# Performance work log

Measured on AMD Instinct MI355X. Metric: run time of the kernel, lower is better.

## Reference

```python
import jax, jax.numpy as jnp
import numpy as np
import math

# BilateralDenoiser(influence=1.0): sigma = max(1.0*2, 1e-4) = 2.0
SIGMA = 2.0
RAD = math.ceil(SIGMA * 2.5)   # 5 -> 11x11 window (N = 2*RAD+1)
EPS = 1e-4
B, H, W = 1, 1080, 1920


def setup_inputs() -> dict:
    key = jax.random.key(0)
    # [B,H,W,8] = color(3) | normal(3) | z(1) | dz(1); rand keeps z,dz positive
    x = jax.random.uniform(key, (B, H, W, 8), dtype=jnp.float32)
    return {"input": x}


def _denoise(inp):
    col = inp[..., 0:3]
    n = inp[..., 3:6]
    # util.safe_normalize: x / sqrt(clamp(dot(x,x), min=1e-20))
    nrm = n * jax.lax.rsqrt(jnp.clip(jnp.sum(n * n, -1, keepdims=True), 1e-20, None))
    z = inp[..., 6:7]
    dz = inp[..., 7:8]

    pad = ((0, 0), (RAD, RAD), (RAD, RAD), (0, 0))
    col_p = jnp.pad(col, pad)
    nrm_p = jnp.pad(nrm, pad)
    z_p = jnp.pad(z, pad)
    m_p = jnp.pad(jnp.ones_like(z), pad)  # validity mask: out-of-image taps get w=0
    var = jnp.float32(SIGMA * SIGMA)

    def row(carry, dy):
        acc_c, acc_w = carry
        for dx in range(-RAD, RAD + 1):  # fixed 11-wide unroll, vectorized over B,H,W
            start = (0, dy + RAD, dx + RAD, 0)
            t_c = jax.lax.dynamic_slice(col_p, start, (B, H, W, 3))
            t_n = jax.lax.dynamic_slice(nrm_p, start, (B, H, W, 3))
            t_z = jax.lax.dynamic_slice(z_p, start, (B, H, W, 1))
            t_m = jax.lax.dynamic_slice(m_p, start, (B, H, W, 1))
            d2 = (dy * dy + dx * dx).astype(jnp.float32)
            w_xy = jnp.exp(-d2 / (2.0 * var))                      # spatial gaussian
            w_n = jnp.clip(jnp.sum(t_n * nrm, -1, keepdims=True), 0.0, 1.0) ** 128  # normal similarity
            w_d = jnp.exp(-jnp.abs(t_z - z) / jnp.maximum(dz * jnp.sqrt(d2), EPS))  # depth similarity
            wgt = w_xy * w_n * w_d * t_m
            acc_c = acc_c + t_c * wgt
            acc_w = acc_w + wgt
        return (acc_c, acc_w), None

    dys = jnp.arange(-RAD, RAD + 1, dtype=jnp.int32)
    init = (jnp.zeros_like(col), jnp.zeros_like(z))
    (s_c, s_w), _ = jax.lax.scan(row, init, dys)
    # center tap always has weight 1 -> s_w >= 1, safe division
    return s_c / s_w


def reference(input):
    return _denoise(input)
```

## Files before the change

kernel.cpp:

```cpp
#include <hip/hip_runtime.h>
#include <math.h>

#define HH 1080
#define WW 1920
#define RAD 5
#define TX 32
#define TY 16
#define RPT 2
#define BDY 8
#define LR (TY + 2*RAD)
#define LC (TX + 2*RAD)

__device__ __forceinline__ float fast_rcp(float x) {
#if __has_builtin(__builtin_amdgcn_rcpf)
    return __builtin_amdgcn_rcpf(x);
#else
    return 1.0f / x;
#endif
}
__device__ __forceinline__ float fast_rsq(float x) {
#if __has_builtin(__builtin_amdgcn_rsqf)
    return __builtin_amdgcn_rsqf(x);
#else
    return rsqrtf(x);
#endif
}
__device__ __forceinline__ float fast_exp2(float x) {
#if __has_builtin(__builtin_amdgcn_exp2f)
    return __builtin_amdgcn_exp2f(x);
#else
    return exp2f(x);
#endif
}


__global__ __launch_bounds__(TX*BDY, 4)
void denoise_kernel(const float* __restrict__ in, float* __restrict__ out) {
    __shared__ float4 sA[LR][LC];
    __shared__ float2 sN[LR][LC];
    __shared__ float  sZ[LR][LC];

    const int tx = threadIdx.x;
    const int ty = threadIdx.y;
    const int tid = ty * TX + tx;
    const int x0 = blockIdx.x * TX;
    const int y0 = blockIdx.y * TY;

    #pragma unroll
    for (int i = 0; i < (LR * LC + TX * BDY - 1) / (TX * BDY); ++i) {
        int idx = tid + i * (TX * BDY);
        if (idx < LR * LC) {
            int r = idx / LC, c = idx % LC;
            int gx = x0 + c - RAD;
            int gy = y0 + r - RAD;
            float4 a = make_float4(0.f, 0.f, 0.f, 0.f);
            float4 b = make_float4(0.f, 0.f, 0.f, 0.f);
            if ((unsigned)gx < (unsigned)WW && (unsigned)gy < (unsigned)HH) {
                const float4* p = reinterpret_cast<const float4*>(in + ((size_t)gy * WW + gx) * 8);
                a = p[0];
                b = p[1];
            }
            float nn = a.w * a.w + b.x * b.x + b.y * b.y;
            float s = fast_rsq(fmaxf(nn, 1e-20f));
            sA[r][c] = make_float4(a.x, a.y, a.z, a.w * s);
            sN[r][c] = make_float2(b.x * s, b.y * s);
            sZ[r][c] = b.z;
        }
    }
    __syncthreads();

    float cn0[RPT], cn1[RPT], cn2[RPT], cz[RPT], rdz[RPT];
    #pragma unroll
    for (int o = 0; o < RPT; ++o) {
        int rr = ty * RPT + RAD + o, cc = tx + RAD;
        float4 A = sA[rr][cc];
        float2 N = sN[rr][cc];
        cn0[o] = A.w; cn1[o] = N.x; cn2[o] = N.y; cz[o] = sZ[rr][cc];
        int gy = y0 + ty * RPT + o;
        float dzv = 1.0f;
        if (gy < HH) dzv = in[(((size_t)gy * WW) + (x0 + tx)) * 8 + 7];
        rdz[o] = fminf(1.4426950408889634f * fast_rcp(dzv), 1e10f);
    }
    const float rr1 = rdz[1] * fast_rcp(rdz[0]);

    float accx[RPT] = {0.f, 0.f};
    float accy[RPT] = {0.f, 0.f};
    float accz[RPT] = {0.f, 0.f};
    float accw[RPT] = {0.f, 0.f};

    float tmu0[RAD + 1] = {}, tmu1[RAD + 1] = {};

    #define ROW_BODY(CHECK)                                                          \
    {                                                                                \
        _Pragma("unroll")                                                            \
        for (int k = 0; k <= RAD; ++k) tmu1[k] = tmu0[k] * rr1;                      \
        if (!CHECK || r <= 2 * RAD) {   \
            int dy0 = r - RAD;                                                      \
            float dy0sq = (float)(dy0 * dy0);                                       \
            _Pragma("unroll")                                                       \
            for (int k = 0; k <= RAD; ++k)                                          \
                tmu0[k] = rdz[0] * fast_rsq(dy0sq + (float)(k * k));                \
        }                                                                            \
        float tmv[RPT][RAD + 1], cxv[RPT][RAD + 1];                                  \
        bool  val[RPT];                                                              \
        _Pragma("unroll")                                                            \
        for (int o = 0; o < RPT; ++o) {                                              \
            int dy = r - RAD - o;                                                    \
            val[o] = (dy >= -RAD) && (dy <= RAD);                                    \
            if (!CHECK || val[o]) {                                                  \
                float dy2f = (float)(dy * dy);                                       \
                float bneg = fmaf(dy2f, -0.18033688011112042f, -276.997447850681f);  \
                _Pragma("unroll")                                                    \
                for (int k = 0; k <= RAD; ++k) {                                     \
                    float tmuk = (o == 0) ? tmu0[k] : tmu1[k];                       \
                    cxv[o][k] = bneg + (float)(k * k) * -0.18033688011112042f;       \
                    tmv[o][k] = fminf(tmuk, 14426.950408889634f);                    \
                }                                                                    \
            }                                                                        \
        }                                                                            \
        _Pragma("unroll")                                                            \
        for (int dx = 0; dx < 2 * RAD + 1; ++dx) {                                   \
            float4 A  = sA[ty * RPT + r][tx + dx];                                   \
            float2 N  = sN[ty * RPT + r][tx + dx];                                   \
            float  tz = sZ[ty * RPT + r][tx + dx];                                   \
            const int k = (dx < RAD) ? (RAD - dx) : (dx - RAD);                      \
            _Pragma("unroll")                                                        \
            for (int o = 0; o < RPT; ++o) {                                          \
                if (!CHECK || val[o]) {                                              \
                    float dot = fmaf(A.w, cn0[o], fmaf(N.x, cn1[o], N.y * cn2[o]));  \
                    float vv  = fmaf(dot, -92.332482616893665f, 369.32993046757466f); \
                    float zd  = tz - cz[o];                                          \
                    float e2a = fmaf(-fabsf(zd), tmv[o][k], cxv[o][k]);              \
                    float e2  = fmaf(dot, vv, e2a);                                  \
                    float w   = fast_exp2(e2);                                       \
                    accx[o] = fmaf(A.x, w, accx[o]);                                 \
                    accy[o] = fmaf(A.y, w, accy[o]);                                 \
                    accz[o] = fmaf(A.z, w, accz[o]);                                 \
                    accw[o] += w;                                                    \
                }                                                                    \
            }                                                                        \
        }                                                                            \
    }

    #pragma unroll 1
    for (int r = 0; r < RPT - 1; ++r) ROW_BODY(true)
    #pragma unroll 1
    for (int r = RPT - 1; r <= 2 * RAD; ++r) ROW_BODY(false)
    #pragma unroll 1
    for (int r = 2 * RAD + 1; r < 2 * RAD + RPT; ++r) ROW_BODY(true)

    #undef ROW_BODY

    const int xo = x0 + tx;
    #pragma unroll
    for (int o = 0; o < RPT; ++o) {
        int y = y0 + ty * RPT + o;
        if (y < HH) {
            float inv = fast_rcp(accw[o]);
            size_t base = ((size_t)y * WW + xo) * 3;
            out[base + 0] = accx[o] * inv;
            out[base + 1] = accy[o] * inv;
            out[base + 2] = accz[o] * inv;
        }
    }
}

extern "C" void kernel_launch(void* const* d_in, const int* in_sizes, int n_in,
                              void* d_out, int out_size, void* d_ws, size_t ws_size,
                              hipStream_t stream) {
    const float* in = (const float*)d_in[0];
    float* out = (float*)d_out;
    dim3 grid((WW + TX - 1) / TX, (HH + TY - 1) / TY);
    dim3 block(TX, BDY);
    hipLaunchKernelGGL(denoise_kernel, grid, block, 0, stream, in, out);
}
```

Measured before the change: 106.2 us.

## Pack horizontal taps into float2 vectors for packed FMA and split shared arrays

```diff
diff --git a/kernel.cpp b/kernel.cpp
--- a/kernel.cpp
+++ b/kernel.cpp
@@ -11,6 +11,8 @@
 #define LR (TY + 2*RAD)
 #define LC (TX + 2*RAD)
 
+typedef float f32x2 __attribute__((ext_vector_type(2)));
+
 __device__ __forceinline__ float fast_rcp(float x) {
 #if __has_builtin(__builtin_amdgcn_rcpf)
     return __builtin_amdgcn_rcpf(x);
@@ -32,13 +34,21 @@
     return exp2f(x);
 #endif
 }
-
+__device__ __forceinline__ f32x2 splat(float v) { f32x2 r; r.x = v; r.y = v; return r; }
+
+
+#define NCf   (-0.18033688011112042f)
+#define CBf   (-276.997447850681f)
+#define PAf   (-92.332482616893665f)
+#define PBf   (369.32993046757466f)
+#define BIGT  (14426.950408889634f)
+#define K25NC (25.0f * NCf)
 
 __global__ __launch_bounds__(TX*BDY, 4)
 void denoise_kernel(const float* __restrict__ in, float* __restrict__ out) {
-    __shared__ float4 sA[LR][LC];
-    __shared__ float2 sN[LR][LC];
-    __shared__ float  sZ[LR][LC];
+    __shared__ float sC0[LR][LC], sC1[LR][LC], sC2[LR][LC];
+    __shared__ float sN0[LR][LC], sN1[LR][LC], sN2[LR][LC];
+    __shared__ float sZv[LR][LC];
 
     const int tx = threadIdx.x;
     const int ty = threadIdx.y;
@@ -62,31 +72,39 @@
             }
             float nn = a.w * a.w + b.x * b.x + b.y * b.y;
             float s = fast_rsq(fmaxf(nn, 1e-20f));
-            sA[r][c] = make_float4(a.x, a.y, a.z, a.w * s);
-            sN[r][c] = make_float2(b.x * s, b.y * s);
-            sZ[r][c] = b.z;
+            sC0[r][c] = a.x; sC1[r][c] = a.y; sC2[r][c] = a.z;
+            sN0[r][c] = a.w * s; sN1[r][c] = b.x * s; sN2[r][c] = b.y * s;
+            sZv[r][c] = b.z;
         }
     }
     __syncthreads();
 
-    float cn0[RPT], cn1[RPT], cn2[RPT], cz[RPT], rdz[RPT];
+    f32x2 cn0p[RPT], cn1p[RPT], cn2p[RPT], czp[RPT];
+    float rdz[RPT];
     #pragma unroll
     for (int o = 0; o < RPT; ++o) {
         int rr = ty * RPT + RAD + o, cc = tx + RAD;
-        float4 A = sA[rr][cc];
-        float2 N = sN[rr][cc];
-        cn0[o] = A.w; cn1[o] = N.x; cn2[o] = N.y; cz[o] = sZ[rr][cc];
+        cn0p[o] = splat(sN0[rr][cc]);
+        cn1p[o] = splat(sN1[rr][cc]);
+        cn2p[o] = splat(sN2[rr][cc]);
+        czp[o]  = splat(sZv[rr][cc]);
         int gy = y0 + ty * RPT + o;
         float dzv = 1.0f;
         if (gy < HH) dzv = in[(((size_t)gy * WW) + (x0 + tx)) * 8 + 7];
         rdz[o] = fminf(1.4426950408889634f * fast_rcp(dzv), 1e10f);
     }
     const float rr1 = rdz[1] * fast_rcp(rdz[0]);
-
-    float accx[RPT] = {0.f, 0.f};
-    float accy[RPT] = {0.f, 0.f};
-    float accz[RPT] = {0.f, 0.f};
-    float accw[RPT] = {0.f, 0.f};
+    const f32x2 PAp = splat(PAf), PBp = splat(PBf);
+    const f32x2 K2C[5] = { {25.f*NCf, 16.f*NCf}, {9.f*NCf, 4.f*NCf}, {NCf, 0.0f},
+                           {NCf, 4.f*NCf},       {9.f*NCf, 16.f*NCf} };
+
+    f32x2 ax2[RPT], ay2[RPT], az2[RPT], aw2[RPT];
+    float sxl[RPT], syl[RPT], szl[RPT], swl[RPT];
+    #pragma unroll
+    for (int o = 0; o < RPT; ++o) {
+        ax2[o] = splat(0.f); ay2[o] = splat(0.f); az2[o] = splat(0.f); aw2[o] = splat(0.f);
+        sxl[o] = syl[o] = szl[o] = swl[o] = 0.f;
+    }
 
     float tmu0[RAD + 1] = {}, tmu1[RAD + 1] = {};
 
@@ -94,49 +112,85 @@
     {                                                                                \
         _Pragma("unroll")                                                            \
         for (int k = 0; k <= RAD; ++k) tmu1[k] = tmu0[k] * rr1;                      \
-        if (!CHECK || r <= 2 * RAD) {   \
-            int dy0 = r - RAD;                                                      \
-            float dy0sq = (float)(dy0 * dy0);                                       \
-            _Pragma("unroll")                                                       \
-            for (int k = 0; k <= RAD; ++k)                                          \
-                tmu0[k] = rdz[0] * fast_rsq(dy0sq + (float)(k * k));                \
-        }                                                                            \
-        float tmv[RPT][RAD + 1], cxv[RPT][RAD + 1];                                  \
+        if (!CHECK || r <= 2 * RAD) {                                                \
+            int dy0 = r - RAD;                                                       \
+            float dy0sq = (float)(dy0 * dy0);                                        \
+            _Pragma("unroll")                                                        \
+            for (int k = 0; k <= RAD; ++k)                                           \
+                tmu0[k] = rdz[0] * fast_rsq(dy0sq + (float)(k * k));                 \
+        }                                                                            \
+        constexpr int JK0[5] = {5, 3, 1, 1, 3};                                      \
+        constexpr int JK1[5] = {4, 2, 0, 2, 4};                                      \
         bool  val[RPT];                                                              \
+        f32x2 tm2v[RPT][5], bneg2[RPT];                                              \
+        float tm5[RPT];                                                              \
         _Pragma("unroll")                                                            \
         for (int o = 0; o < RPT; ++o) {                                              \
             int dy = r - RAD - o;                                                    \
             val[o] = (dy >= -RAD) && (dy <= RAD);                                    \
             if (!CHECK || val[o]) {                                                  \
                 float dy2f = (float)(dy * dy);                                       \
-                float bneg = fmaf(dy2f, -0.18033688011112042f, -276.997447850681f);  \
+                bneg2[o] = splat(fmaf(dy2f, NCf, CBf));                              \
                 _Pragma("unroll")                                                    \
-                for (int k = 0; k <= RAD; ++k) {                                     \
-                    float tmuk = (o == 0) ? tmu0[k] : tmu1[k];                       \
-                    cxv[o][k] = bneg + (float)(k * k) * -0.18033688011112042f;       \
-                    tmv[o][k] = fminf(tmuk, 14426.950408889634f);                    \
+                for (int j = 0; j < 5; ++j) {                                        \
+                    float ta = (o == 0) ? tmu0[JK0[j]] : tmu1[JK0[j]];               \
+                    float tb = (o == 0) ? tmu0[JK1[j]] : tmu1[JK1[j]];               \
+                    tm2v[o][j].x = fminf(ta, BIGT);                                  \
+                    tm2v[o][j].y = fminf(tb, BIGT);                                  \
                 }                                                                    \
+                tm5[o] = fminf((o == 0) ? tmu0[5] : tmu1[5], BIGT);                  \
             }                                                                        \
         }                                                                            \
+        const int rr_ = ty * RPT + r;                                                \
         _Pragma("unroll")                                                            \
-        for (int dx = 0; dx < 2 * RAD + 1; ++dx) {                                   \
-            float4 A  = sA[ty * RPT + r][tx + dx];                                   \
-            float2 N  = sN[ty * RPT + r][tx + dx];                                   \
-            float  tz = sZ[ty * RPT + r][tx + dx];                                   \
-            const int k = (dx < RAD) ? (RAD - dx) : (dx - RAD);                      \
+        for (int j = 0; j < 5; ++j) {                                                \
+            const int cA = tx + 2 * j, cB = cA + 1;                                  \
+            f32x2 pC0 = {sC0[rr_][cA], sC0[rr_][cB]};                                \
+            f32x2 pC1 = {sC1[rr_][cA], sC1[rr_][cB]};                                \
+            f32x2 pC2 = {sC2[rr_][cA], sC2[rr_][cB]};                                \
+            f32x2 pN0 = {sN0[rr_][cA], sN0[rr_][cB]};                                \
+            f32x2 pN1 = {sN1[rr_][cA], sN1[rr_][cB]};                                \
+            f32x2 pN2 = {sN2[rr_][cA], sN2[rr_][cB]};                                \
+            f32x2 pZ  = {sZv[rr_][cA], sZv[rr_][cB]};                                \
             _Pragma("unroll")                                                        \
             for (int o = 0; o < RPT; ++o) {                                          \
                 if (!CHECK || val[o]) {                                              \
-                    float dot = fmaf(A.w, cn0[o], fmaf(N.x, cn1[o], N.y * cn2[o]));  \
-                    float vv  = fmaf(dot, -92.332482616893665f, 369.32993046757466f); \
-                    float zd  = tz - cz[o];                                          \
-                    float e2a = fmaf(-fabsf(zd), tmv[o][k], cxv[o][k]);              \
-                    float e2  = fmaf(dot, vv, e2a);                                  \
-                    float w   = fast_exp2(e2);                                       \
-                    accx[o] = fmaf(A.x, w, accx[o]);                                 \
-                    accy[o] = fmaf(A.y, w, accy[o]);                                 \
-                    accz[o] = fmaf(A.z, w, accz[o]);                                 \
-                    accw[o] += w;                                                    \
+                    f32x2 dd = __builtin_elementwise_fma(pN0, cn0p[o],               \
+                                __builtin_elementwise_fma(pN1, cn1p[o],              \
+                                                          pN2 * cn2p[o]));           \
+                    f32x2 vv = __builtin_elementwise_fma(dd, PAp, PBp);              \
+                    f32x2 zd = pZ - czp[o];                                          \
+                    f32x2 zb; zb.x = fabsf(zd.x); zb.y = fabsf(zd.y);                \
+                    f32x2 cx2 = K2C[j] + bneg2[o];                                   \
+                    f32x2 ea = __builtin_elementwise_fma(-zb, tm2v[o][j], cx2);      \
+                    f32x2 e2 = __builtin_elementwise_fma(dd, vv, ea);                \
+                    f32x2 w2; w2.x = fast_exp2(e2.x); w2.y = fast_exp2(e2.y);        \
+                    ax2[o] = __builtin_elementwise_fma(pC0, w2, ax2[o]);             \
+                    ay2[o] = __builtin_elementwise_fma(pC1, w2, ay2[o]);             \
+                    az2[o] = __builtin_elementwise_fma(pC2, w2, az2[o]);             \
+                    aw2[o] = aw2[o] + w2;                                            \
+                }                                                                    \
+            }                                                                        \
+        }                                                                            \
+        {    \
+            const int cL = tx + 10;                                                  \
+            float C0s = sC0[rr_][cL], C1s = sC1[rr_][cL], C2s = sC2[rr_][cL];        \
+            float N0s = sN0[rr_][cL], N1s = sN1[rr_][cL], N2s = sN2[rr_][cL];        \
+            float Zs  = sZv[rr_][cL];                                                \
+            _Pragma("unroll")                                                        \
+            for (int o = 0; o < RPT; ++o) {                                          \
+                if (!CHECK || val[o]) {                                              \
+                    float dot = fmaf(N0s, cn0p[o].x, fmaf(N1s, cn1p[o].x, N2s * cn2p[o].x)); \
+                    float vvs = fmaf(dot, PAf, PBf);                                 \
+                    float zds = Zs - czp[o].x;                                       \
+                    float cxs = bneg2[o].x + K25NC;                                  \
+                    float eas = fmaf(-fabsf(zds), tm5[o], cxs);                      \
+                    float e2s = fmaf(dot, vvs, eas);                                 \
+                    float ws  = fast_exp2(e2s);                                      \
+                    sxl[o] = fmaf(C0s, ws, sxl[o]);                                  \
+                    syl[o] = fmaf(C1s, ws, syl[o]);                                  \
+                    szl[o] = fmaf(C2s, ws, szl[o]);                                  \
+                    swl[o] += ws;                                                    \
                 }                                                                    \
             }                                                                        \
         }                                                                            \
@@ -156,11 +210,15 @@
     for (int o = 0; o < RPT; ++o) {
         int y = y0 + ty * RPT + o;
         if (y < HH) {
-            float inv = fast_rcp(accw[o]);
+            float tw = aw2[o].x + aw2[o].y + swl[o];
+            float txc = ax2[o].x + ax2[o].y + sxl[o];
+            float tyc = ay2[o].x + ay2[o].y + syl[o];
+            float tzc = az2[o].x + az2[o].y + szl[o];
+            float inv = fast_rcp(tw);
             size_t base = ((size_t)y * WW + xo) * 3;
-            out[base + 0] = accx[o] * inv;
-            out[base + 1] = accy[o] * inv;
-            out[base + 2] = accz[o] * inv;
+            out[base + 0] = txc * inv;
+            out[base + 1] = tyc * inv;
+            out[base + 2] = tzc * inv;
         }
     }
 }
```

After: 113.4 us. +6.8%, slower.
